# Kernel tuning notes

Hardware: AMD Instinct MI355X
Metric: run time of the kernel (lower is better)

## Reference

```python
import jax, jax.numpy as jnp
import numpy as np

B, S, D = 8, 1024, 768
H = 12
DH = D // H  # 64


def setup_inputs() -> dict:
    key = jax.random.key(0)
    k1, k2 = jax.random.split(key)
    x = jax.random.normal(k1, (B, S, D), dtype=jnp.float32)
    attention_mask = jnp.zeros((B, 1, 1, S), dtype=jnp.float32)
    W = jax.random.normal(k2, (D, D), dtype=jnp.float32) * (1.0 / np.sqrt(D))
    b = jnp.zeros((D,), dtype=jnp.float32)
    return {"x": x, "attention_mask": attention_mask, "W": W, "b": b}


def reference(x, attention_mask, W, b):
    # Linear projection (torch Linear: y = x @ W^T + b; here W is [out,in])
    mixed = jnp.einsum('bsd,ed->bse', x, W) + b            # [B,S,D]
    # split heads -> [B,H,S,DH]
    xl = mixed.reshape(B, S, H, DH).transpose(0, 2, 1, 3)
    # self-attention with Q=K=V=xl
    scores = jnp.einsum('bhsd,bhtd->bhst', xl, xl) / jnp.sqrt(
        jnp.asarray(DH, dtype=xl.dtype))                    # [B,H,S,S]
    scores = scores + attention_mask
    probs = jax.nn.softmax(scores, axis=-1)
    ctx = jnp.einsum('bhst,bhtd->bhsd', probs, xl)          # [B,H,S,DH]
    ctx = ctx.transpose(0, 2, 1, 3).reshape(B, S, D)        # [B,S,D]
    return ctx
```

## Files before the change

### kernel.cpp

```cpp
#include <hip/hip_runtime.h>
#include <hip/hip_bf16.h>


#define D_MODEL 768
#define SEQ     1024
#define NHEAD   12
#define DHEAD   64
#define BATCH   8
#define QB      128
#define LOG2E   1.44269504088896f
#define FMLOG   28.8539008178f
#define SCLC    (0.125f * LOG2E)

typedef __attribute__((ext_vector_type(8)))  short bf16x8;
typedef __attribute__((ext_vector_type(4)))  short short4v;
typedef __attribute__((ext_vector_type(4)))  float f32x4;
typedef __attribute__((ext_vector_type(16))) float f32x16;

__device__ __forceinline__ unsigned short f2bf(float f) {
  __hip_bfloat16 h = __float2bfloat16(f);
  return *reinterpret_cast<unsigned short*>(&h);
}

__device__ __forceinline__ float fexp2(float x) {
#if __has_builtin(__builtin_amdgcn_exp2f)
  return __builtin_amdgcn_exp2f(x);
#else
  return exp2f(x);
#endif
}

__device__ __forceinline__ int lswz(int r, int c) {
  return (r << 6) + (c ^ ((r & 7) << 3));
}
__device__ __forceinline__ int tau(int t) {
  return (t & ~0xC) | ((t & 8) >> 1) | ((t & 4) << 1);
}

template<bool WRITE_T>
__global__ __launch_bounds__(256) void proj_kernel(
    const float* __restrict__ X, const float* __restrict__ W,
    const float* __restrict__ bias, unsigned short* __restrict__ mixed,
    unsigned short* __restrict__ mixedT)
{
  __shared__ unsigned short As[2][64 * 40];
  __shared__ unsigned short Bs[2][128 * 40];

  const int tid = threadIdx.x;
  const int l   = tid & 63;
  const int w   = tid >> 6;
  const int m0  = blockIdx.x * 64;
  const int n0  = blockIdx.y * 128;
  const int wm  = (w >> 1) * 32;
  const int wn  = (w & 1) * 64;
  const int lr  = l & 15;
  const int g   = l >> 4;
  const int lk  = g * 8;

  const int ar = tid >> 2;
  const int ac = (tid & 3) * 8;

  f32x4 a0, a1, b0[2], b1[2];
  auto loadSlab = [&](int k0) {
    const float* pa = &X[(size_t)(m0 + ar) * D_MODEL + k0 + ac];
    a0 = *(const f32x4*)pa;
    a1 = *(const f32x4*)(pa + 4);
    #pragma unroll
    for (int p = 0; p < 2; ++p) {
      const float* pb = &W[(size_t)(n0 + ar + p * 64) * D_MODEL + k0 + ac];
      b0[p] = *(const f32x4*)pb;
      b1[p] = *(const f32x4*)(pb + 4);
    }
  };
  auto stageSlab = [&](int bb) {
    bf16x8 av;
    #pragma unroll
    for (int jj = 0; jj < 4; ++jj) {
      av[jj]     = (short)f2bf(a0[jj]);
      av[4 + jj] = (short)f2bf(a1[jj]);
    }
    *(bf16x8*)&As[bb][ar * 40 + ac] = av;
    #pragma unroll
    for (int p = 0; p < 2; ++p) {
      bf16x8 bv;
      #pragma unroll
      for (int jj = 0; jj < 4; ++jj) {
        bv[jj]     = (short)f2bf(b0[p][jj]);
        bv[4 + jj] = (short)f2bf(b1[p][jj]);
      }
      *(bf16x8*)&Bs[bb][(ar + p * 64) * 40 + ac] = bv;
    }
  };

  f32x4 acc[2][4] = {};

  loadSlab(0);
  stageSlab(0);
  __syncthreads();

  int cur = 0;
  for (int k0 = 0; k0 < D_MODEL; k0 += 32) {
    const bool more = (k0 + 32 < D_MODEL);
    if (more) loadSlab(k0 + 32);

    bf16x8 af[2], bfr[4];
    #pragma unroll
    for (int am = 0; am < 2; ++am)
      af[am]  = *(const bf16x8*)&As[cur][(wm + am * 16 + lr) * 40 + lk];
    #pragma unroll
    for (int bn = 0; bn < 4; ++bn)
      bfr[bn] = *(const bf16x8*)&Bs[cur][(wn + bn * 16 + lr) * 40 + lk];

    #pragma unroll
    for (int am = 0; am < 2; ++am)
      #pragma unroll
      for (int bn = 0; bn < 4; ++bn)
        acc[am][bn] = __builtin_amdgcn_mfma_f32_16x16x32_bf16(
            af[am], bfr[bn], acc[am][bn], 0, 0, 0);

    if (more) {
      stageSlab(cur ^ 1);
      __syncthreads();
    }
    cur ^= 1;
  }

  const int orow = g * 4;
  const int bT   = m0 >> 10;
  const int tl0  = (m0 & 1023) + wm + orow;
  #pragma unroll
  for (int bn = 0; bn < 4; ++bn) {
    int   col  = n0 + wn + bn * 16 + lr;
    float bcol = bias[col];
    size_t tbase = ((size_t)bT * D_MODEL + col) * SEQ;
    #pragma unroll
    for (int am = 0; am < 2; ++am) {
      short4v pk;
      #pragma unroll
      for (int i = 0; i < 4; ++i) {
        float v = acc[am][bn][i] + bcol;
        unsigned short hv = f2bf(v);
        mixed[(size_t)(m0 + wm + am * 16 + orow + i) * D_MODEL + col] = hv;
        pk[i] = (short)hv;
      }
      if (WRITE_T)
        *(short4v*)&mixedT[tbase + tau(tl0 + am * 16)] = pk;
    }
  }
}

template<bool PRE_T>
__global__ __launch_bounds__(256, 4) void attn_kernel(
    const unsigned short* __restrict__ mixed,
    const unsigned short* __restrict__ mixedT,
    const float* __restrict__ mask, float* __restrict__ out)
{
  __shared__ unsigned short Xbuf[2][4096];
  __shared__ unsigned short Tbuf[2][4096];
  __shared__ float maskE[SEQ];
  __shared__ float lb[128];
  __shared__ int   mflag;

  const int tid = threadIdx.x;
  const int l   = tid & 63;
  const int wq  = tid >> 6;
  const int l31 = l & 31;
  const int lh  = l >> 5;
  const int h4  = lh * 4;
  const int h8  = lh * 8;

  const int id  = blockIdx.x;
  const int xcd = id & 7;
  const int j   = id >> 3;
  const int pr  = xcd * 12 + (j >> 3);
  const int q0  = (j & 7) * QB;
  const int hd  = pr % NHEAD;
  const int b   = pr / NHEAD;

  const size_t base  = ((size_t)b * SEQ) * D_MODEL + hd * DHEAD;
  const size_t baseT = ((size_t)b * D_MODEL + hd * DHEAD) * SEQ;

  const int r0 = tid >> 3;
  const int sc = (tid & 7) * 8;

  if (tid == 0) mflag = 0;
  __syncthreads();
  {
    f32x4 mv = *(const f32x4*)&mask[(size_t)b * SEQ + tid * 4];
    #pragma unroll
    for (int jj = 0; jj < 4; ++jj)
      maskE[tid * 4 + jj] = fmaf(mv[jj], LOG2E, -FMLOG);
    if (mv[0] != 0.f || mv[1] != 0.f || mv[2] != 0.f || mv[3] != 0.f)
      mflag = 1;
  }

  unsigned short* QQ = &Xbuf[0][0];
  #pragma unroll
  for (int pp = 0; pp < 4; ++pp) {
    int g   = tid + pp * 256;
    int row = g >> 3;
    int c   = (g & 7) * 8;
    *(bf16x8*)&QQ[lswz(row, c)] =
        *(const bf16x8*)&mixed[base + (size_t)(q0 + row) * D_MODEL + c];
  }
  __syncthreads();

  const bool hm = (mflag != 0);
  bf16x8 qf[4];
  #pragma unroll
  for (int db = 0; db < 4; ++db)
    qf[db] = *(const bf16x8*)&QQ[lswz(wq * 32 + l31, db * 16 + h8)];
  __syncthreads();

  bf16x8 k0r, k1r, t0r, t1r;
  auto loadKV = [&](int tt) {
    k0r = *(const bf16x8*)&mixed[base + (size_t)(tt + r0) * D_MODEL + sc];
    k1r = *(const bf16x8*)&mixed[base + (size_t)(tt + r0 + 32) * D_MODEL + sc];
    if (PRE_T) {
      t0r = *(const bf16x8*)&mixedT[baseT + (size_t)r0 * SEQ + tt + sc];
      t1r = *(const bf16x8*)&mixedT[baseT + (size_t)(r0 + 32) * SEQ + tt + sc];
    }
  };
  auto stageKV = [&](unsigned short* Xd, unsigned short* Td) {
    *(bf16x8*)&Xd[lswz(r0, sc)]      = k0r;
    *(bf16x8*)&Xd[lswz(r0 + 32, sc)] = k1r;
    if (PRE_T) {
      *(bf16x8*)&Td[lswz(r0, sc)]      = t0r;
      *(bf16x8*)&Td[lswz(r0 + 32, sc)] = t1r;
    } else {
      int tl0 = tau(r0), tl1 = tau(r0 + 32);
      #pragma unroll
      for (int jj = 0; jj < 8; ++jj) {
        Td[lswz(sc + jj, tl0)] = (unsigned short)k0r[jj];
        Td[lswz(sc + jj, tl1)] = (unsigned short)k1r[jj];
      }
    }
  };

  unsigned short* Xc = &Xbuf[0][0];
  unsigned short* Xn = &Xbuf[1][0];
  unsigned short* Tc = &Tbuf[0][0];
  unsigned short* Tn = &Tbuf[1][0];

  loadKV(0);
  stageKV(Xc, Tc);
  __syncthreads();

  f32x16 c0 = {}, c1 = {};
  float lsum = 0.f;

  for (int t0 = 0; t0 < SEQ; t0 += 64) {
    const bool more = (t0 + 64 < SEQ);
    if (more) loadKV(t0 + 64);

    #pragma unroll
    for (int sub = 0; sub < 2; ++sub) {
      const int sr = sub * 32;

      f32x16 s = {};
      #pragma unroll
      for (int db = 0; db < 4; ++db) {
        bf16x8 kf = *(const bf16x8*)&Xc[lswz(sr + l31, db * 16 + h8)];
        s = __builtin_amdgcn_mfma_f32_32x32x16_bf16(kf, qf[db], s, 0, 0, 0);
      }

      float p[16];
      if (hm) {
        #pragma unroll
        for (int r = 0; r < 16; ++r) {
          int kvr = (r & 3) + 8 * (r >> 2) + h4;
          p[r] = fexp2(fmaf(s[r], SCLC, maskE[t0 + sr + kvr]));
          lsum += p[r];
        }
      } else {
        #pragma unroll
        for (int r = 0; r < 16; ++r) {
          p[r] = fexp2(fmaf(s[r], SCLC, -FMLOG));
          lsum += p[r];
        }
      }

      #pragma unroll
      for (int f = 0; f < 2; ++f) {
        bf16x8 pa;
        #pragma unroll
        for (int jj = 0; jj < 8; ++jj) pa[jj] = (short)f2bf(p[8 * f + jj]);
        const int cc = sr + f * 16 + h8;
        bf16x8 v0 = *(const bf16x8*)&Tc[lswz(l31, cc)];
        bf16x8 v1 = *(const bf16x8*)&Tc[lswz(32 + l31, cc)];
        c0 = __builtin_amdgcn_mfma_f32_32x32x16_bf16(pa, v0, c0, 0, 0, 0);
        c1 = __builtin_amdgcn_mfma_f32_32x32x16_bf16(pa, v1, c1, 0, 0, 0);
      }
    }

    if (more) {
      stageKV(Xn, Tn);
      __syncthreads();
    }
    unsigned short* t;
    t = Xc; Xc = Xn; Xn = t;
    t = Tc; Tc = Tn; Tn = t;
  }

  float l_tot = lsum + __shfl_xor(lsum, 32);
  if (lh == 0) lb[wq * 32 + l31] = l_tot;

  #pragma unroll
  for (int r = 0; r < 16; ++r) {
    int qr = (r & 3) + 8 * (r >> 2) + h4;
    float linv = __builtin_amdgcn_rcpf(lb[wq * 32 + qr]);
    int row = q0 + wq * 32 + qr;
    float* orow = &out[((size_t)b * SEQ + row) * D_MODEL + hd * DHEAD];
    orow[l31]      = c0[r] * linv;
    orow[32 + l31] = c1[r] * linv;
  }
}

extern "C" void kernel_launch(void* const* d_in, const int* in_sizes, int n_in,
                              void* d_out, int out_size, void* d_ws, size_t ws_size,
                              hipStream_t stream) {
  const float* x    = (const float*)d_in[0];
  const float* mask = (const float*)d_in[1];
  const float* W    = (const float*)d_in[2];
  const float* bias = (const float*)d_in[3];
  float* out        = (float*)d_out;

  const size_t NM = (size_t)8192 * D_MODEL;
  unsigned short* mixed  = (unsigned short*)d_ws;
  unsigned short* mixedT = mixed + NM;
  const size_t need = NM * 2 * 2;
  const bool preT = ws_size >= need;

  dim3 gp(8192 / 64, D_MODEL / 128);
  const int nblk = (SEQ / QB) * NHEAD * BATCH;

  if (preT) {
    proj_kernel<true><<<gp, 256, 0, stream>>>(x, W, bias, mixed, mixedT);
    attn_kernel<true><<<nblk, 256, 0, stream>>>(mixed, mixedT, mask, out);
  } else {
    proj_kernel<false><<<gp, 256, 0, stream>>>(x, W, bias, mixed, mixed);
    attn_kernel<false><<<nblk, 256, 0, stream>>>(mixed, mixed, mask, out);
  }
}
```

Before: 67.41 us.

## Use two waves per attention block, each handling 64 query rows

The attention kernel now runs 128 threads (two waves) per 128-query block instead of four waves. Each wave owns two 32-row query tiles, so every K fragment read from LDS feeds two QK MFMAs and every V fragment feeds four PV MFMAs, which roughly halves LDS reads per MFMA. The next-tile global prefetch is moved after the softmax of the first sub-tile, and the fallback path without a pretransposed V is removed. In exchange, register pressure rises and there are fewer waves per CU to hide latency, and the kernel now assumes the workspace is large enough for the transposed copy.

```diff
diff --git a/kernel.cpp b/kernel.cpp
--- a/kernel.cpp
+++ b/kernel.cpp
@@ -149,21 +149,20 @@
   }
 }
 
-template<bool PRE_T>
-__global__ __launch_bounds__(256, 4) void attn_kernel(
+__global__ __launch_bounds__(128) void attn_kernel(
     const unsigned short* __restrict__ mixed,
     const unsigned short* __restrict__ mixedT,
     const float* __restrict__ mask, float* __restrict__ out)
 {
-  __shared__ unsigned short Xbuf[2][4096];
-  __shared__ unsigned short Tbuf[2][4096];
+  __shared__ unsigned short Kbuf[2][4096];
+  __shared__ unsigned short Vbuf[2][4096];
   __shared__ float maskE[SEQ];
   __shared__ float lb[128];
   __shared__ int   mflag;
 
   const int tid = threadIdx.x;
   const int l   = tid & 63;
-  const int wq  = tid >> 6;
+  const int w   = tid >> 6;
   const int l31 = l & 31;
   const int lh  = l >> 5;
   const int h4  = lh * 4;
@@ -186,18 +185,22 @@
   if (tid == 0) mflag = 0;
   __syncthreads();
   {
-    f32x4 mv = *(const f32x4*)&mask[(size_t)b * SEQ + tid * 4];
-    #pragma unroll
-    for (int jj = 0; jj < 4; ++jj)
-      maskE[tid * 4 + jj] = fmaf(mv[jj], LOG2E, -FMLOG);
-    if (mv[0] != 0.f || mv[1] != 0.f || mv[2] != 0.f || mv[3] != 0.f)
+    f32x4 m0 = *(const f32x4*)&mask[(size_t)b * SEQ + tid * 8];
+    f32x4 m1 = *(const f32x4*)&mask[(size_t)b * SEQ + tid * 8 + 4];
+    #pragma unroll
+    for (int jj = 0; jj < 4; ++jj) {
+      maskE[tid * 8 + jj]     = fmaf(m0[jj], LOG2E, -FMLOG);
+      maskE[tid * 8 + 4 + jj] = fmaf(m1[jj], LOG2E, -FMLOG);
+    }
+    if (m0[0] != 0.f || m0[1] != 0.f || m0[2] != 0.f || m0[3] != 0.f ||
+        m1[0] != 0.f || m1[1] != 0.f || m1[2] != 0.f || m1[3] != 0.f)
       mflag = 1;
   }
 
-  unsigned short* QQ = &Xbuf[0][0];
+  unsigned short* QQ = &Kbuf[0][0];
   #pragma unroll
-  for (int pp = 0; pp < 4; ++pp) {
-    int g   = tid + pp * 256;
+  for (int pp = 0; pp < 8; ++pp) {
+    int g   = tid + pp * 128;
     int row = g >> 3;
     int c   = (g & 7) * 8;
     *(bf16x8*)&QQ[lswz(row, c)] =
@@ -206,113 +209,145 @@
   __syncthreads();
 
   const bool hm = (mflag != 0);
-  bf16x8 qf[4];
+  bf16x8 qfA[4], qfB[4];
   #pragma unroll
-  for (int db = 0; db < 4; ++db)
-    qf[db] = *(const bf16x8*)&QQ[lswz(wq * 32 + l31, db * 16 + h8)];
-  __syncthreads();
-
-  bf16x8 k0r, k1r, t0r, t1r;
+  for (int db = 0; db < 4; ++db) {
+    qfA[db] = *(const bf16x8*)&QQ[lswz(w * 64 + l31,      db * 16 + h8)];
+    qfB[db] = *(const bf16x8*)&QQ[lswz(w * 64 + 32 + l31, db * 16 + h8)];
+  }
+  __syncthreads();
+
+  bf16x8 kr[4], vr[4];
   auto loadKV = [&](int tt) {
-    k0r = *(const bf16x8*)&mixed[base + (size_t)(tt + r0) * D_MODEL + sc];
-    k1r = *(const bf16x8*)&mixed[base + (size_t)(tt + r0 + 32) * D_MODEL + sc];
-    if (PRE_T) {
-      t0r = *(const bf16x8*)&mixedT[baseT + (size_t)r0 * SEQ + tt + sc];
-      t1r = *(const bf16x8*)&mixedT[baseT + (size_t)(r0 + 32) * SEQ + tt + sc];
+    #pragma unroll
+    for (int p = 0; p < 4; ++p) {
+      kr[p] = *(const bf16x8*)&mixed[base + (size_t)(tt + r0 + p * 16) * D_MODEL + sc];
+      vr[p] = *(const bf16x8*)&mixedT[baseT + (size_t)(r0 + p * 16) * SEQ + tt + sc];
     }
   };
-  auto stageKV = [&](unsigned short* Xd, unsigned short* Td) {
-    *(bf16x8*)&Xd[lswz(r0, sc)]      = k0r;
-    *(bf16x8*)&Xd[lswz(r0 + 32, sc)] = k1r;
-    if (PRE_T) {
-      *(bf16x8*)&Td[lswz(r0, sc)]      = t0r;
-      *(bf16x8*)&Td[lswz(r0 + 32, sc)] = t1r;
-    } else {
-      int tl0 = tau(r0), tl1 = tau(r0 + 32);
-      #pragma unroll
-      for (int jj = 0; jj < 8; ++jj) {
-        Td[lswz(sc + jj, tl0)] = (unsigned short)k0r[jj];
-        Td[lswz(sc + jj, tl1)] = (unsigned short)k1r[jj];
-      }
+  auto stageKV = [&](unsigned short* Kd, unsigned short* Vd) {
+    #pragma unroll
+    for (int p = 0; p < 4; ++p) {
+      *(bf16x8*)&Kd[lswz(r0 + p * 16, sc)] = kr[p];
+      *(bf16x8*)&Vd[lswz(r0 + p * 16, sc)] = vr[p];
     }
   };
 
-  unsigned short* Xc = &Xbuf[0][0];
-  unsigned short* Xn = &Xbuf[1][0];
-  unsigned short* Tc = &Tbuf[0][0];
-  unsigned short* Tn = &Tbuf[1][0];
+  unsigned short* Kc = &Kbuf[0][0];
+  unsigned short* Kn = &Kbuf[1][0];
+  unsigned short* Vc = &Vbuf[0][0];
+  unsigned short* Vn = &Vbuf[1][0];
 
   loadKV(0);
-  stageKV(Xc, Tc);
-  __syncthreads();
-
-  f32x16 c0 = {}, c1 = {};
-  float lsum = 0.f;
+  stageKV(Kc, Vc);
+  __syncthreads();
+
+  f32x16 c0A = {}, c1A = {}, c0B = {}, c1B = {};
+  float lsA = 0.f, lsB = 0.f;
 
   for (int t0 = 0; t0 < SEQ; t0 += 64) {
     const bool more = (t0 + 64 < SEQ);
-    if (more) loadKV(t0 + 64);
 
     #pragma unroll
     for (int sub = 0; sub < 2; ++sub) {
       const int sr = sub * 32;
 
-      f32x16 s = {};
+      f32x16 sA = {}, sB = {};
       #pragma unroll
       for (int db = 0; db < 4; ++db) {
-        bf16x8 kf = *(const bf16x8*)&Xc[lswz(sr + l31, db * 16 + h8)];
-        s = __builtin_amdgcn_mfma_f32_32x32x16_bf16(kf, qf[db], s, 0, 0, 0);
-      }
-
-      float p[16];
-      if (hm) {
+        bf16x8 kf = *(const bf16x8*)&Kc[lswz(sr + l31, db * 16 + h8)];
+        sA = __builtin_amdgcn_mfma_f32_32x32x16_bf16(kf, qfA[db], sA, 0, 0, 0);
+        sB = __builtin_amdgcn_mfma_f32_32x32x16_bf16(kf, qfB[db], sB, 0, 0, 0);
+      }
+
+      bf16x8 paA[2], paB[2];
+      {
+        float p[16];
+        if (hm) {
+          #pragma unroll
+          for (int r = 0; r < 16; ++r) {
+            int kvr = (r & 3) + 8 * (r >> 2) + h4;
+            p[r] = fexp2(fmaf(sA[r], SCLC, maskE[t0 + sr + kvr]));
+            lsA += p[r];
+          }
+        } else {
+          #pragma unroll
+          for (int r = 0; r < 16; ++r) {
+            p[r] = fexp2(fmaf(sA[r], SCLC, -FMLOG));
+            lsA += p[r];
+          }
+        }
         #pragma unroll
-        for (int r = 0; r < 16; ++r) {
-          int kvr = (r & 3) + 8 * (r >> 2) + h4;
-          p[r] = fexp2(fmaf(s[r], SCLC, maskE[t0 + sr + kvr]));
-          lsum += p[r];
+        for (int f = 0; f < 2; ++f)
+          #pragma unroll
+          for (int jj = 0; jj < 8; ++jj) paA[f][jj] = (short)f2bf(p[8 * f + jj]);
+      }
+      {
+        float p[16];
+        if (hm) {
+          #pragma unroll
+          for (int r = 0; r < 16; ++r) {
+            int kvr = (r & 3) + 8 * (r >> 2) + h4;
+            p[r] = fexp2(fmaf(sB[r], SCLC, maskE[t0 + sr + kvr]));
+            lsB += p[r];
+          }
+        } else {
+          #pragma unroll
+          for (int r = 0; r < 16; ++r) {
+            p[r] = fexp2(fmaf(sB[r], SCLC, -FMLOG));
+            lsB += p[r];
+          }
         }
-      } else {
         #pragma unroll
-        for (int r = 0; r < 16; ++r) {
-          p[r] = fexp2(fmaf(s[r], SCLC, -FMLOG));
-          lsum += p[r];
-        }
-      }
+        for (int f = 0; f < 2; ++f)
+          #pragma unroll
+          for (int jj = 0; jj < 8; ++jj) paB[f][jj] = (short)f2bf(p[8 * f + jj]);
+      }
+
+      if (sub == 0 && more) loadKV(t0 + 64);
 
       #pragma unroll
       for (int f = 0; f < 2; ++f) {
-        bf16x8 pa;
-        #pragma unroll
-        for (int jj = 0; jj < 8; ++jj) pa[jj] = (short)f2bf(p[8 * f + jj]);
         const int cc = sr + f * 16 + h8;
-        bf16x8 v0 = *(const bf16x8*)&Tc[lswz(l31, cc)];
-        bf16x8 v1 = *(const bf16x8*)&Tc[lswz(32 + l31, cc)];
-        c0 = __builtin_amdgcn_mfma_f32_32x32x16_bf16(pa, v0, c0, 0, 0, 0);
-        c1 = __builtin_amdgcn_mfma_f32_32x32x16_bf16(pa, v1, c1, 0, 0, 0);
+        bf16x8 v0 = *(const bf16x8*)&Vc[lswz(l31, cc)];
+        bf16x8 v1 = *(const bf16x8*)&Vc[lswz(32 + l31, cc)];
+        c0A = __builtin_amdgcn_mfma_f32_32x32x16_bf16(paA[f], v0, c0A, 0, 0, 0);
+        c1A = __builtin_amdgcn_mfma_f32_32x32x16_bf16(paA[f], v1, c1A, 0, 0, 0);
+        c0B = __builtin_amdgcn_mfma_f32_32x32x16_bf16(paB[f], v0, c0B, 0, 0, 0);
+        c1B = __builtin_amdgcn_mfma_f32_32x32x16_bf16(paB[f], v1, c1B, 0, 0, 0);
       }
     }
 
     if (more) {
-      stageKV(Xn, Tn);
+      stageKV(Kn, Vn);
       __syncthreads();
     }
     unsigned short* t;
-    t = Xc; Xc = Xn; Xn = t;
-    t = Tc; Tc = Tn; Tn = t;
-  }
-
-  float l_tot = lsum + __shfl_xor(lsum, 32);
-  if (lh == 0) lb[wq * 32 + l31] = l_tot;
+    t = Kc; Kc = Kn; Kn = t;
+    t = Vc; Vc = Vn; Vn = t;
+  }
+
+  float ltA = lsA + __shfl_xor(lsA, 32);
+  float ltB = lsB + __shfl_xor(lsB, 32);
+  if (lh == 0) {
+    lb[w * 64 + l31]      = ltA;
+    lb[w * 64 + 32 + l31] = ltB;
+  }
 
   #pragma unroll
   for (int r = 0; r < 16; ++r) {
     int qr = (r & 3) + 8 * (r >> 2) + h4;
-    float linv = __builtin_amdgcn_rcpf(lb[wq * 32 + qr]);
-    int row = q0 + wq * 32 + qr;
-    float* orow = &out[((size_t)b * SEQ + row) * D_MODEL + hd * DHEAD];
-    orow[l31]      = c0[r] * linv;
-    orow[32 + l31] = c1[r] * linv;
+    int rowA = q0 + w * 64 + qr;
+    float liA = __builtin_amdgcn_rcpf(lb[w * 64 + qr]);
+    float* oA = &out[((size_t)b * SEQ + rowA) * D_MODEL + hd * DHEAD];
+    oA[l31]      = c0A[r] * liA;
+    oA[32 + l31] = c1A[r] * liA;
+
+    int rowB = rowA + 32;
+    float liB = __builtin_amdgcn_rcpf(lb[w * 64 + 32 + qr]);
+    float* oB = &out[((size_t)b * SEQ + rowB) * D_MODEL + hd * DHEAD];
+    oB[l31]      = c0B[r] * liB;
+    oB[32 + l31] = c1B[r] * liB;
   }
 }
 
@@ -328,17 +363,10 @@
   const size_t NM = (size_t)8192 * D_MODEL;
   unsigned short* mixed  = (unsigned short*)d_ws;
   unsigned short* mixedT = mixed + NM;
-  const size_t need = NM * 2 * 2;
-  const bool preT = ws_size >= need;
 
   dim3 gp(8192 / 64, D_MODEL / 128);
   const int nblk = (SEQ / QB) * NHEAD * BATCH;
 
-  if (preT) {
-    proj_kernel<true><<<gp, 256, 0, stream>>>(x, W, bias, mixed, mixedT);
-    attn_kernel<true><<<nblk, 256, 0, stream>>>(mixed, mixedT, mask, out);
-  } else {
-    proj_kernel<false><<<gp, 256, 0, stream>>>(x, W, bias, mixed, mixed);
-    attn_kernel<false><<<nblk, 256, 0, stream>>>(mixed, mixed, mask, out);
-  }
-}
+  proj_kernel<true><<<gp, 256, 0, stream>>>(x, W, bias, mixed, mixedT);
+  attn_kernel<<<nblk, 128, 0, stream>>>(mixed, mixedT, mask, out);
+}
```

After: 94.47 us. 1.4x slower.
